# Performance work log

Hardware: AMD Instinct MI355X
Metric: run time of the kernel (lower is better)

## Reference

```python
import jax, jax.numpy as jnp
import numpy as np

N, K, D = 65536, 1024, 512
INIT_COUNT = 100


def setup_inputs() -> dict:
    key = jax.random.key(0)
    k1, k2 = jax.random.split(key)
    embedded = jax.random.normal(k1, (N, D), dtype=jnp.float32)
    centers = jax.random.normal(k2, (K, D), dtype=jnp.float32)
    count = jnp.full((K,), INIT_COUNT, dtype=jnp.int32)  # start_training: ones(K)*100
    return {"embedded": embedded, "centers": centers, "count": count}


def reference(embedded, centers, count):
    # --- squared_euclidean_distance(centers, embedded): dist[n,k] = ||e_n - c_k||^2 ---
    e2 = jnp.sum(embedded * embedded, axis=-1, keepdims=True)   # [N,1]
    c2 = jnp.sum(centers * centers, axis=-1)                    # [K]
    cross = embedded @ centers.T                                # [N,K] GEMM
    dist = e2 + c2[None, :] - 2.0 * cross                       # [N,K]

    # compression_loss: min over clusters, then mean
    loss = jnp.mean(jnp.min(dist, axis=1))

    # prediction_hard: hard assignments
    s = jnp.argmin(dist, axis=1)                                # [N] int

    # update_centroids: the per-sample EMA with eta = 1/count[c] is exactly an
    # incremental (running) mean seeded with `count` pseudo-counts, so the
    # sequential loop is mathematically equivalent to a vectorized segment mean:
    #   new_centers[c] = (count[c]*centers[c] + sum_{s_i=c} e_i) / (count[c] + n_c)
    added = jax.ops.segment_sum(embedded, s, num_segments=K)                       # [K,D]
    n_add = jax.ops.segment_sum(jnp.ones_like(s, dtype=jnp.int32), s, num_segments=K)  # [K]
    new_count = count + n_add
    cf = count.astype(centers.dtype)[:, None]
    new_centers = (cf * centers + added) / new_count.astype(centers.dtype)[:, None]

    return loss, s, new_centers, new_count
```

## Files before the change

kernel.cpp:

```cpp
#include <hip/hip_runtime.h>

#define N_SAMPLES 65536
#define K_CENT    1024
#define DIM       512
#define TAU 0.125f

typedef __attribute__((ext_vector_type(8))) short  short8;
typedef _Float16 half8 __attribute__((ext_vector_type(8)));
typedef __attribute__((ext_vector_type(4))) float  float4v;

__device__ inline unsigned short f2h_bits(float x) {
    _Float16 h = (_Float16)x;
    return __builtin_bit_cast(unsigned short, h);
}

__global__ __launch_bounds__(256) void pack_kernel(const float* __restrict__ cen,
                                                   unsigned short* __restrict__ Bp,
                                                   float* __restrict__ c2) {
    const int wv = threadIdx.x >> 6, lane = threadIdx.x & 63;
    const int k = blockIdx.x * 4 + wv;
    const int kk = lane >> 2, quad = lane & 3;
    const float* src = cen + (size_t)k * DIM + kk * 32 + quad * 8;
    float4 v0 = *(const float4*)src;
    float4 v1 = *(const float4*)(src + 4);
    float f[8] = {v0.x, v0.y, v0.z, v0.w, v1.x, v1.y, v1.z, v1.w};
    short8 h;
    float s = 0.f;
    #pragma unroll
    for (int e = 0; e < 8; ++e) { h[e] = (short)f2h_bits(f[e]); s += f[e] * f[e]; }
    const int ntG = k >> 7, j4 = (k >> 4) & 7, l15 = k & 15;
    size_t slot = (size_t)(ntG * 16 + kk) * 512 + j4 * 64 + quad * 16 + l15;
    *(short8*)(Bp + slot * 8) = h;
    for (int off = 32; off; off >>= 1) s += __shfl_down(s, off);
    if (lane == 0) c2[k] = s;
}

__device__ inline void loadA(const float* aBase, int kc, float4v av[2][2]) {
    #pragma unroll
    for (int i = 0; i < 2; ++i) {
        const float4v* ap = (const float4v*)(aBase + (size_t)i * 16 * DIM + kc);
        av[i][0] = ap[0];
        av[i][1] = ap[1];
    }
}

__device__ inline void cvtA1(const float4v av[2][2], half8 ah[2]) {
    #pragma unroll
    for (int i = 0; i < 2; ++i) {
        #pragma unroll
        for (int e = 0; e < 8; ++e)
            ah[i][e] = (_Float16)av[i][e >> 2][e & 3];
    }
}

__global__ __launch_bounds__(256, 2) void assign_mfma(
    const float* __restrict__ A,
    const unsigned short* __restrict__ Bp,
    const float* __restrict__ c2,
    float* __restrict__ pbest,
    float* __restrict__ psec,
    int* __restrict__ pidx)
{
    __shared__ float st_best[128];
    __shared__ float st_sec[128];
    __shared__ int   st_idx[128];

    const int tid  = threadIdx.x;
    const int w    = tid >> 6;
    const int lane = tid & 63;
    const int quad = lane >> 4;
    const int l15  = lane & 15;
    const int m0   = blockIdx.x * 128;

    if (tid < 128) { st_best[tid] = 3.4e38f; st_sec[tid] = 3.4e38f; st_idx[tid] = 0; }
    __syncthreads();

    const float* aBase = A + (size_t)(m0 + w * 32 + l15) * DIM + quad * 8;

    short8 br[2][8];
    float4v avN[2][2];
    half8 ah[2];

    #pragma unroll
    for (int j = 0; j < 8; ++j)
        br[0][j] = *(const short8*)(Bp + j * 512 + lane * 8);
    loadA(aBase, 0, avN);
    cvtA1(avN, ah);

    for (int nt = 0; nt < 8; ++nt) {
        const int n0 = nt * 128;

        float4v acc[16];
        #pragma unroll
        for (int z = 0; z < 16; ++z) acc[z] = (float4v){0.f, 0.f, 0.f, 0.f};

        #pragma unroll
        for (int ks = 0; ks < 16; ++ks) {
            const int s   = nt * 16 + ks;
            const int cur = ks & 1;
            const int nxt = cur ^ 1;

            {
                const int sN = (s < 127) ? s + 1 : 127;
                const unsigned short* bkN = Bp + (size_t)sN * 4096;
                #pragma unroll
                for (int j = 0; j < 8; ++j)
                    br[nxt][j] = *(const short8*)(bkN + j * 512 + lane * 8);
                loadA(aBase, ((ks + 1) & 15) * 32, avN);
            }

            #pragma unroll
            for (int j4 = 0; j4 < 8; ++j4) {
                half8 bh = __builtin_bit_cast(half8, br[cur][j4]);
                acc[0 * 8 + j4] = __builtin_amdgcn_mfma_f32_16x16x32_f16(
                    ah[0], bh, acc[0 * 8 + j4], 0, 0, 0);
                acc[1 * 8 + j4] = __builtin_amdgcn_mfma_f32_16x16x32_f16(
                    ah[1], bh, acc[1 * 8 + j4], 0, 0, 0);
            }

            cvtA1(avN, ah);
        }

        float c2v[8];
        #pragma unroll
        for (int j = 0; j < 8; ++j) c2v[j] = c2[n0 + j * 16 + l15];
        #pragma unroll
        for (int i = 0; i < 2; ++i)
            #pragma unroll
            for (int reg = 0; reg < 4; ++reg) {
                float bv = 3.4e38f, sv = 3.4e38f; int bi = 0;
                #pragma unroll
                for (int j = 0; j < 8; ++j) {
                    float v = c2v[j] - 2.0f * acc[i * 8 + j][reg];
                    int n = n0 + j * 16 + l15;
                    if (v < bv) { sv = bv; bv = v; bi = n; }
                    else if (v < sv) sv = v;
                }
                #pragma unroll
                for (int mask = 1; mask < 16; mask <<= 1) {
                    float ob = __shfl_xor(bv, mask);
                    float os = __shfl_xor(sv, mask);
                    int   oi = __shfl_xor(bi, mask);
                    float ns = fminf(fminf(sv, os), fmaxf(bv, ob));
                    if (ob < bv || (ob == bv && oi < bi)) { bv = ob; bi = oi; }
                    sv = ns;
                }
                if (l15 == 0) {
                    int ml = w * 32 + i * 16 + quad * 4 + reg;
                    float sb = st_best[ml], ss = st_sec[ml]; int si = st_idx[ml];
                    float ns = fminf(fminf(ss, sv), fmaxf(sb, bv));
                    if (bv < sb || (bv == sb && bi < si)) { st_best[ml] = bv; st_idx[ml] = bi; }
                    st_sec[ml] = ns;
                }
            }
    }

    __syncthreads();
    if (tid < 128) {
        int m = m0 + tid;
        pbest[m] = st_best[tid];
        psec [m] = st_sec[tid];
        pidx [m] = st_idx[tid];
    }
}

__global__ __launch_bounds__(256) void merge_kernel(
    const float* __restrict__ pbest,
    const float* __restrict__ psec,
    const int* __restrict__ pidx,
    int* __restrict__ s_idx,
    float* __restrict__ out_s,
    int* __restrict__ hist,
    int* __restrict__ flag_cnt,
    int* __restrict__ flagged,
    double* __restrict__ loss_d)
{
    int m = blockIdx.x * 256 + threadIdx.x;
    float bv = pbest[m];
    float sv = psec[m];
    int   bi = pidx[m];
    s_idx[m] = bi;
    out_s[m] = (float)bi;
    atomicAdd(&hist[bi], 1);
    if (sv - bv < TAU) { int p = atomicAdd(flag_cnt, 1); flagged[p] = m; }

    float ls = bv;
    for (int off = 32; off; off >>= 1) ls += __shfl_down(ls, off);
    __shared__ float ws4[4];
    int lane = threadIdx.x & 63, wv = threadIdx.x >> 6;
    if (lane == 0) ws4[wv] = ls;
    __syncthreads();
    if (threadIdx.x == 0)
        atomicAdd(loss_d, (double)(ws4[0] + ws4[1] + ws4[2] + ws4[3]));
}

__global__ __launch_bounds__(256) void refine_kernel(
    const float* __restrict__ emb,
    const float* __restrict__ cen,
    const int* __restrict__ flag_cnt,
    const int* __restrict__ flagged,
    int* __restrict__ s_idx,
    float* __restrict__ out_s,
    int* __restrict__ hist)
{
    __shared__ float e_sh[DIM];
    __shared__ double rvd[256];
    __shared__ int rid[256];
    const int t = threadIdx.x;
    const int cnt = *flag_cnt;
    for (int idx = blockIdx.x; idx < cnt; idx += gridDim.x) {
        int n = flagged[idx];
        __syncthreads();
        ((float2*)e_sh)[t] = ((const float2*)(emb + (size_t)n * DIM))[t];
        __syncthreads();
        double bestd = 1e300;
        int bestk = 0;
        #pragma unroll
        for (int j = 0; j < 4; ++j) {
            int k = t * 4 + j;
            const float* crow = cen + (size_t)k * DIM;
            double acc = 0.0;
            for (int d = 0; d < DIM; d += 4) {
                float4 cv = *(const float4*)(crow + d);
                double d0 = (double)e_sh[d + 0] - (double)cv.x;
                double d1 = (double)e_sh[d + 1] - (double)cv.y;
                double d2 = (double)e_sh[d + 2] - (double)cv.z;
                double d3 = (double)e_sh[d + 3] - (double)cv.w;
                acc += d0 * d0 + d1 * d1 + d2 * d2 + d3 * d3;
            }
            if (acc < bestd) { bestd = acc; bestk = k; }
        }
        rvd[t] = bestd; rid[t] = bestk;
        __syncthreads();
        for (int off = 128; off; off >>= 1) {
            if (t < off) {
                double v = rvd[t + off]; int ii = rid[t + off];
                if (v < rvd[t] || (v == rvd[t] && ii < rid[t])) { rvd[t] = v; rid[t] = ii; }
            }
            __syncthreads();
        }
        if (t == 0) {
            int old = s_idx[n], nw = rid[0];
            if (nw != old) {
                atomicSub(&hist[old], 1);
                atomicAdd(&hist[nw], 1);
                s_idx[n] = nw;
                out_s[n] = (float)nw;
            }
        }
    }
}

__global__ void scan_kernel(const int* __restrict__ hist,
                            int* __restrict__ offsets,
                            int* __restrict__ cursor,
                            const int* __restrict__ count_in,
                            float* __restrict__ out_count) {
    __shared__ int sbuf[K_CENT];
    int t = threadIdx.x;
    int v = hist[t];
    sbuf[t] = v;
    __syncthreads();
    for (int off = 1; off < K_CENT; off <<= 1) {
        int x = (t >= off) ? sbuf[t - off] : 0;
        __syncthreads();
        sbuf[t] += x;
        __syncthreads();
    }
    int incl = sbuf[t];
    offsets[t] = incl - v;
    cursor[t]  = incl - v;
    out_count[t] = (float)(count_in[t] + v);
    if (t == K_CENT - 1) offsets[K_CENT] = incl;
}

__global__ void scatter_kernel(const int* __restrict__ s_idx,
                               int* __restrict__ cursor,
                               int* __restrict__ order) {
    int n = blockIdx.x * blockDim.x + threadIdx.x;
    if (n < N_SAMPLES) {
        int pos = atomicAdd(&cursor[s_idx[n]], 1);
        order[pos] = n;
    }
}

__global__ __launch_bounds__(256) void gp_kernel(
    const float* __restrict__ emb,
    const int* __restrict__ s_idx,
    const int* __restrict__ order,
    float* __restrict__ accum,
    double* __restrict__ loss_d)
{
    __shared__ int s_n[64], s_c[64];
    const int t = threadIdx.x;
    const int base = blockIdx.x * 64;
    if (t < 64) { int n = order[base + t]; s_n[t] = n; s_c[t] = s_idx[n]; }
    __syncthreads();
    float ax = 0.f, ay = 0.f, ssq = 0.f;
    int cur = s_c[0];
    for (int r = 0; r < 64; ++r) {
        int n = s_n[r], c = s_c[r];
        if (c != cur) {
            atomicAdd(&accum[(size_t)cur * DIM + t * 2], ax);
            atomicAdd(&accum[(size_t)cur * DIM + t * 2 + 1], ay);
            ax = ay = 0.f; cur = c;
        }
        float2 e = *(const float2*)(emb + (size_t)n * DIM + t * 2);
        ax += e.x; ay += e.y;
        ssq += e.x * e.x + e.y * e.y;
    }
    atomicAdd(&accum[(size_t)cur * DIM + t * 2], ax);
    atomicAdd(&accum[(size_t)cur * DIM + t * 2 + 1], ay);

    for (int off = 32; off; off >>= 1) ssq += __shfl_down(ssq, off);
    __shared__ float wsum[4];
    if ((t & 63) == 0) wsum[t >> 6] = ssq;
    __syncthreads();
    if (t == 0)
        atomicAdd(loss_d, (double)(wsum[0] + wsum[1] + wsum[2] + wsum[3]));
}

__global__ __launch_bounds__(256) void combine_kernel(
    const float* __restrict__ centers,
    const int* __restrict__ count_in,
    const int* __restrict__ hist,
    const float* __restrict__ accum,
    const double* __restrict__ loss_d,
    float* __restrict__ out_centers,
    float* __restrict__ out_loss)
{
    int k = blockIdx.x, t = threadIdx.x;
    if (k == 0 && t == 0) *out_loss = (float)(*loss_d * (1.0 / N_SAMPLES));
    float cn = (float)count_in[k];
    float tot = cn + (float)hist[k];
    float2 c = *(const float2*)(centers + (size_t)k * DIM + t * 2);
    float2 a = *(const float2*)(accum   + (size_t)k * DIM + t * 2);
    float2 o;
    o.x = (cn * c.x + a.x) / tot;
    o.y = (cn * c.y + a.y) / tot;
    *(float2*)(out_centers + (size_t)k * DIM + t * 2) = o;
}

extern "C" void kernel_launch(void* const* d_in, const int* in_sizes, int n_in,
                              void* d_out, int out_size, void* d_ws, size_t ws_size,
                              hipStream_t stream) {
    const float* emb = (const float*)d_in[0];
    const float* cen = (const float*)d_in[1];
    const int*   cnt = (const int*)d_in[2];

    float* out = (float*)d_out;
    float* out_loss    = out;
    float* out_s       = out + 1;
    float* out_centers = out + 1 + N_SAMPLES;
    float* out_count   = out + 1 + N_SAMPLES + (size_t)K_CENT * DIM;

    int* wsi = (int*)d_ws;
    int*   hist     = wsi;
    int*   offsets  = wsi + 1024;
    int*   cursor   = wsi + 2064;
    int*   s_idx    = wsi + 4096;
    float* c2       = (float*)(wsi + 69632);
    int*   flag_cnt = wsi + 70656;
    double* loss_d  = (double*)(wsi + 70712);
    int*   flagged  = wsi + 70720;
    float* pbest    = (float*)(wsi + 136256);
    float* psec     = (float*)(wsi + 267328);
    int*   pidx     = wsi + 398400;
    unsigned short* Bp = (unsigned short*)(wsi + 529472);
    int*   order    = wsi + 136256;
    float* accum    = (float*)(wsi + 529472);

    hipMemsetAsync(hist, 0, K_CENT * sizeof(int), stream);
    hipMemsetAsync(loss_d, 0, sizeof(double), stream);
    hipMemsetAsync(flag_cnt, 0, sizeof(int), stream);

    pack_kernel<<<256, 256, 0, stream>>>(cen, Bp, c2);
    assign_mfma<<<512, 256, 0, stream>>>(emb, Bp, c2, pbest, psec, pidx);
    merge_kernel<<<N_SAMPLES / 256, 256, 0, stream>>>(pbest, psec, pidx, s_idx, out_s,
                                                      hist, flag_cnt, flagged, loss_d);
    hipMemsetAsync(accum, 0, (size_t)K_CENT * DIM * sizeof(float), stream);
    refine_kernel<<<256, 256, 0, stream>>>(emb, cen, flag_cnt, flagged, s_idx, out_s, hist);
    scan_kernel<<<1, K_CENT, 0, stream>>>(hist, offsets, cursor, cnt, out_count);
    scatter_kernel<<<N_SAMPLES / 256, 256, 0, stream>>>(s_idx, cursor, order);
    gp_kernel<<<N_SAMPLES / 64, 256, 0, stream>>>(emb, s_idx, order, accum, loss_d);
    combine_kernel<<<K_CENT, 256, 0, stream>>>(cen, cnt, hist, accum, loss_d,
                                               out_centers, out_loss);
}
```

Baseline: 684.8 us.

## Fuse merge step into assign kernel and manually double-buffer B registers

Folds the merge kernel (index write, histogram atomics, flagging of near-ties, loss reduction) into the epilogue of the MFMA assignment kernel. This removes a launch and the round trip of per-sample best/second/index arrays through global memory. The k-loop is also rewritten as explicit ping-pong over two named register buffers instead of an indexed 2-D array, and the launch bound drops to one block per SM, which allows more registers but may reduce occupancy. Loss reduction now issues one double atomic per wave rather than per block.

```diff
diff --git a/kernel.cpp b/kernel.cpp
--- a/kernel.cpp
+++ b/kernel.cpp
@@ -53,13 +53,36 @@
     }
 }
 
-__global__ __launch_bounds__(256, 2) void assign_mfma(
+#define LOAD_B(dst, sstep)                                                       \
+    {                                                                            \
+        const unsigned short* bk_ = Bp + (size_t)(sstep) * 4096;                 \
+        _Pragma("unroll")                                                        \
+        for (int j_ = 0; j_ < 8; ++j_)                                           \
+            dst[j_] = *(const short8*)(bk_ + j_ * 512 + lane * 8);               \
+    }
+
+#define MFMA_STEP(bsrc)                                                          \
+    {                                                                            \
+        _Pragma("unroll")                                                        \
+        for (int j4_ = 0; j4_ < 8; ++j4_) {                                      \
+            half8 bh_ = __builtin_bit_cast(half8, bsrc[j4_]);                    \
+            acc[j4_]     = __builtin_amdgcn_mfma_f32_16x16x32_f16(               \
+                ah[0], bh_, acc[j4_], 0, 0, 0);                                  \
+            acc[8 + j4_] = __builtin_amdgcn_mfma_f32_16x16x32_f16(               \
+                ah[1], bh_, acc[8 + j4_], 0, 0, 0);                              \
+        }                                                                        \
+    }
+
+__global__ __launch_bounds__(256, 1) void assign_mfma(
     const float* __restrict__ A,
     const unsigned short* __restrict__ Bp,
     const float* __restrict__ c2,
-    float* __restrict__ pbest,
-    float* __restrict__ psec,
-    int* __restrict__ pidx)
+    int* __restrict__ s_idx,
+    float* __restrict__ out_s,
+    int* __restrict__ hist,
+    int* __restrict__ flag_cnt,
+    int* __restrict__ flagged,
+    double* __restrict__ loss_d)
 {
     __shared__ float st_best[128];
     __shared__ float st_sec[128];
@@ -77,47 +100,35 @@
 
     const float* aBase = A + (size_t)(m0 + w * 32 + l15) * DIM + quad * 8;
 
-    short8 br[2][8];
+    short8 brA[8], brB[8];
     float4v avN[2][2];
     half8 ah[2];
 
-    #pragma unroll
-    for (int j = 0; j < 8; ++j)
-        br[0][j] = *(const short8*)(Bp + j * 512 + lane * 8);
+    LOAD_B(brA, 0);
     loadA(aBase, 0, avN);
     cvtA1(avN, ah);
 
     for (int nt = 0; nt < 8; ++nt) {
         const int n0 = nt * 128;
+        const int sBase = nt * 16;
 
         float4v acc[16];
         #pragma unroll
         for (int z = 0; z < 16; ++z) acc[z] = (float4v){0.f, 0.f, 0.f, 0.f};
 
         #pragma unroll
-        for (int ks = 0; ks < 16; ++ks) {
-            const int s   = nt * 16 + ks;
-            const int cur = ks & 1;
-            const int nxt = cur ^ 1;
-
+        for (int ks2 = 0; ks2 < 8; ++ks2) {
+            const int s = sBase + ks2 * 2;
+            LOAD_B(brB, s + 1);
+            loadA(aBase, ((s + 1) & 15) * 32, avN);
+            MFMA_STEP(brA);
+            cvtA1(avN, ah);
             {
-                const int sN = (s < 127) ? s + 1 : 127;
-                const unsigned short* bkN = Bp + (size_t)sN * 4096;
-                #pragma unroll
-                for (int j = 0; j < 8; ++j)
-                    br[nxt][j] = *(const short8*)(bkN + j * 512 + lane * 8);
-                loadA(aBase, ((ks + 1) & 15) * 32, avN);
-            }
-
-            #pragma unroll
-            for (int j4 = 0; j4 < 8; ++j4) {
-                half8 bh = __builtin_bit_cast(half8, br[cur][j4]);
-                acc[0 * 8 + j4] = __builtin_amdgcn_mfma_f32_16x16x32_f16(
-                    ah[0], bh, acc[0 * 8 + j4], 0, 0, 0);
-                acc[1 * 8 + j4] = __builtin_amdgcn_mfma_f32_16x16x32_f16(
-                    ah[1], bh, acc[1 * 8 + j4], 0, 0, 0);
-            }
-
+                const int s2 = (s + 2 < 128) ? s + 2 : 127;
+                LOAD_B(brA, s2);
+            }
+            loadA(aBase, ((s + 2) & 15) * 32, avN);
+            MFMA_STEP(brB);
             cvtA1(avN, ah);
         }
 
@@ -158,40 +169,17 @@
     __syncthreads();
     if (tid < 128) {
         int m = m0 + tid;
-        pbest[m] = st_best[tid];
-        psec [m] = st_sec[tid];
-        pidx [m] = st_idx[tid];
-    }
-}
-
-__global__ __launch_bounds__(256) void merge_kernel(
-    const float* __restrict__ pbest,
-    const float* __restrict__ psec,
-    const int* __restrict__ pidx,
-    int* __restrict__ s_idx,
-    float* __restrict__ out_s,
-    int* __restrict__ hist,
-    int* __restrict__ flag_cnt,
-    int* __restrict__ flagged,
-    double* __restrict__ loss_d)
-{
-    int m = blockIdx.x * 256 + threadIdx.x;
-    float bv = pbest[m];
-    float sv = psec[m];
-    int   bi = pidx[m];
-    s_idx[m] = bi;
-    out_s[m] = (float)bi;
-    atomicAdd(&hist[bi], 1);
-    if (sv - bv < TAU) { int p = atomicAdd(flag_cnt, 1); flagged[p] = m; }
-
-    float ls = bv;
-    for (int off = 32; off; off >>= 1) ls += __shfl_down(ls, off);
-    __shared__ float ws4[4];
-    int lane = threadIdx.x & 63, wv = threadIdx.x >> 6;
-    if (lane == 0) ws4[wv] = ls;
-    __syncthreads();
-    if (threadIdx.x == 0)
-        atomicAdd(loss_d, (double)(ws4[0] + ws4[1] + ws4[2] + ws4[3]));
+        float bv = st_best[tid], sv = st_sec[tid];
+        int   bi = st_idx[tid];
+        s_idx[m] = bi;
+        out_s[m] = (float)bi;
+        atomicAdd(&hist[bi], 1);
+        if (sv - bv < TAU) { int p = atomicAdd(flag_cnt, 1); flagged[p] = m; }
+        float ls = bv;
+        #pragma unroll
+        for (int off = 32; off; off >>= 1) ls += __shfl_down(ls, off);
+        if (lane == 0) atomicAdd(loss_d, (double)ls);
+    }
 }
 
 __global__ __launch_bounds__(256) void refine_kernel(
@@ -363,11 +351,8 @@
     int*   flag_cnt = wsi + 70656;
     double* loss_d  = (double*)(wsi + 70712);
     int*   flagged  = wsi + 70720;
-    float* pbest    = (float*)(wsi + 136256);
-    float* psec     = (float*)(wsi + 267328);
-    int*   pidx     = wsi + 398400;
+    int*   order    = wsi + 136256;
     unsigned short* Bp = (unsigned short*)(wsi + 529472);
-    int*   order    = wsi + 136256;
     float* accum    = (float*)(wsi + 529472);
 
     hipMemsetAsync(hist, 0, K_CENT * sizeof(int), stream);
@@ -375,9 +360,8 @@
     hipMemsetAsync(flag_cnt, 0, sizeof(int), stream);
 
     pack_kernel<<<256, 256, 0, stream>>>(cen, Bp, c2);
-    assign_mfma<<<512, 256, 0, stream>>>(emb, Bp, c2, pbest, psec, pidx);
-    merge_kernel<<<N_SAMPLES / 256, 256, 0, stream>>>(pbest, psec, pidx, s_idx, out_s,
-                                                      hist, flag_cnt, flagged, loss_d);
+    assign_mfma<<<512, 256, 0, stream>>>(emb, Bp, c2, s_idx, out_s,
+                                         hist, flag_cnt, flagged, loss_d);
     hipMemsetAsync(accum, 0, (size_t)K_CENT * DIM * sizeof(float), stream);
     refine_kernel<<<256, 256, 0, stream>>>(emb, cen, flag_cnt, flagged, s_idx, out_s, hist);
     scan_kernel<<<1, K_CENT, 0, stream>>>(hist, offsets, cursor, cnt, out_count);
```

New measurement: 1.031 ms. 1.51x slower.
